# Optimization experiments

Measured on AMD Instinct MI355X. Metric: run time of the kernel, lower is better.

Reference implementation:

```python
import jax, jax.numpy as jnp
import numpy as np

N, K, CIN, COUT = 150000, 27, 32, 64
EPS = 1e-5
NEG_SLOPE = 0.01


def setup_inputs() -> dict:
    key = jax.random.key(0)
    k1, k2, k3, k4, k5, k6 = jax.random.split(key, 6)
    feats = jax.random.normal(k1, (N, CIN), dtype=jnp.float32)
    nbr = jax.random.randint(k2, (N, K), 0, N, dtype=jnp.int32)
    mask = jax.random.randint(k3, (N, K), 0, 2, dtype=jnp.int32).astype(jnp.bool_)
    # per-offset conv weights [K, Cin, Cout], kaiming-ish scale
    W = jax.random.normal(k4, (K, CIN, COUT), dtype=jnp.float32) / np.sqrt(K * CIN)
    gamma = jax.random.normal(k5, (COUT,), dtype=jnp.float32) * 0.1 + 1.0
    beta = jax.random.normal(k6, (COUT,), dtype=jnp.float32) * 0.1
    return {"feats": feats, "W": W, "gamma": gamma, "beta": beta, "nbr": nbr, "mask": mask}


def reference(feats, W, gamma, beta, nbr, mask):
    # sparse conv as gather-GEMM-(implicit scatter): out[n] = sum_k W[k]^T f[nbr[n,k]]
    gathered = jnp.where(mask[..., None], feats[nbr], 0.0)          # [N, K, Cin]
    out = jnp.einsum('nkc,kcd->nd', gathered, W)                     # [N, Cout]
    # BatchNorm over voxel axis (training-mode batch stats)
    mean = jnp.mean(out, axis=0)
    var = jnp.var(out, axis=0)
    out = (out - mean) * jax.lax.rsqrt(var + EPS) * gamma + beta
    # LeakyReLU, negative_slope = 0.01
    return jnp.where(out >= 0, out, NEG_SLOPE * out)
```

## Files before the change

### kernel.cpp

```cpp
#include <hip/hip_runtime.h>

#define N_VOX  150000
#define KNBR   27
#define CIN    32
#define COUT   64
#define NBUCKET 64
#define NEG_SLOPE 0.01f
#define EPS 1e-5f
#define APPLY_BLOCKS 1024
#define VPB 256

typedef __bf16 bf16x8 __attribute__((ext_vector_type(8)));
typedef float  f32x4  __attribute__((ext_vector_type(4)));

#define NB_FEATS 2344
#define NB_W       27
#define NB_Z       32

__global__ __launch_bounds__(256) void prep_all(
    const float* __restrict__ feats, const float* __restrict__ W,
    __bf16* __restrict__ fb, __bf16* __restrict__ Wp,
    float* __restrict__ bsums)
{
    const int t = threadIdx.x;
    int b = blockIdx.x;

    if (b < NB_FEATS) {
        const int i = b * 256 + t;
        if (i < N_VOX * CIN / 8) {
            const float4* p = reinterpret_cast<const float4*>(feats) + (size_t)i * 2;
            const float4 a = p[0], c = p[1];
            bf16x8 o;
            o[0]=(__bf16)a.x; o[1]=(__bf16)a.y; o[2]=(__bf16)a.z; o[3]=(__bf16)a.w;
            o[4]=(__bf16)c.x; o[5]=(__bf16)c.y; o[6]=(__bf16)c.z; o[7]=(__bf16)c.w;
            reinterpret_cast<bf16x8*>(fb)[i] = o;
        }
        return;
    }
    b -= NB_FEATS;

    if (b < NB_W) {
        const int u = b * 256 + t;
        const int lane = u & 63, f = u >> 6;
        const int s = f & 3, k = f >> 2;
        const int n = lane & 15, q = lane >> 4;
        const float* src = W + ((size_t)(k * CIN + q * 8) * COUT + s * 16 + n);
        bf16x8 o;
#pragma unroll
        for (int j = 0; j < 8; ++j) o[j] = (__bf16)src[(size_t)j * COUT];
        reinterpret_cast<bf16x8*>(Wp)[u] = o;
        return;
    }
    b -= NB_W;

    const int z = b * 256 + t;
    if (z < NBUCKET * 2 * COUT) bsums[z] = 0.0f;
}

__global__ __launch_bounds__(256, 2) void conv_mfma5(
    const __bf16* __restrict__ fb,
    const __bf16* __restrict__ Wp,
    const int* __restrict__ nbr,
    const int* __restrict__ mask,
    float* __restrict__ out,
    float* __restrict__ bsums)
{
    __shared__ int idx_s[VPB * KNBR];

    const int t    = threadIdx.x;
    const int base = blockIdx.x * VPB;

    {
        const size_t gb = (size_t)base * KNBR;
        const int vlim  = N_VOX - base;
        const int ilim  = (vlim < VPB ? vlim : VPB) * KNBR;
#pragma unroll
        for (int j = 0; j < KNBR; ++j) {
            const int i = t + 256 * j;
            int v = -1;
            if (i < ilim) v = (mask[gb + i] != 0) ? nbr[gb + i] : -1;
            idx_s[i] = v;
        }
    }
    __syncthreads();

    const int wave = t >> 6;
    const int lane = t & 63;
    const int n16  = lane & 15;
    const int q    = lane >> 4;
    const int wb   = wave * 64;

    const bf16x8* __restrict__ bp = reinterpret_cast<const bf16x8*>(Wp);
    const bf16x8 zv = {};

    const int rr0 = (wb +  0 + n16) * KNBR;
    const int rr1 = (wb + 16 + n16) * KNBR;
    const int rr2 = (wb + 32 + n16) * KNBR;
    const int rr3 = (wb + 48 + n16) * KNBR;

    f32x4 acc[4][4];
#pragma unroll
    for (int a = 0; a < 4; ++a)
#pragma unroll
        for (int b2 = 0; b2 < 4; ++b2) acc[a][b2] = (f32x4){0.f,0.f,0.f,0.f};

    bf16x8 ga[3][4];
    bf16x8 bb[2][4];

#define STAGE_A(K, B) do { \
    const int _i0 = idx_s[rr0 + (K)]; \
    const int _i1 = idx_s[rr1 + (K)]; \
    const int _i2 = idx_s[rr2 + (K)]; \
    const int _i3 = idx_s[rr3 + (K)]; \
    ga[B][0] = *reinterpret_cast<const bf16x8*>(fb + (size_t)(_i0 < 0 ? 0 : _i0) * CIN + q * 8); \
    ga[B][1] = *reinterpret_cast<const bf16x8*>(fb + (size_t)(_i1 < 0 ? 0 : _i1) * CIN + q * 8); \
    ga[B][2] = *reinterpret_cast<const bf16x8*>(fb + (size_t)(_i2 < 0 ? 0 : _i2) * CIN + q * 8); \
    ga[B][3] = *reinterpret_cast<const bf16x8*>(fb + (size_t)(_i3 < 0 ? 0 : _i3) * CIN + q * 8); \
    if (_i0 < 0) ga[B][0] = zv; \
    if (_i1 < 0) ga[B][1] = zv; \
    if (_i2 < 0) ga[B][2] = zv; \
    if (_i3 < 0) ga[B][3] = zv; \
} while (0)

#define STAGE_B(K, B) do { \
    bb[B][0] = bp[((K) * 4 + 0) * 64 + lane]; \
    bb[B][1] = bp[((K) * 4 + 1) * 64 + lane]; \
    bb[B][2] = bp[((K) * 4 + 2) * 64 + lane]; \
    bb[B][3] = bp[((K) * 4 + 3) * 64 + lane]; \
} while (0)

    STAGE_A(0, 0);
    STAGE_B(0, 0);
    STAGE_A(1, 1);
    STAGE_A(2, 2);

#pragma unroll
    for (int k = 0; k < KNBR; ++k) {
        const int cb = k % 3;
        const int db = k & 1;
        if (k + 1 < KNBR) STAGE_B(k + 1, (k + 1) & 1);
#pragma unroll
        for (int s = 0; s < 4; ++s) {
            acc[0][s] = __builtin_amdgcn_mfma_f32_16x16x32_bf16(ga[cb][0], bb[db][s], acc[0][s], 0, 0, 0);
            acc[1][s] = __builtin_amdgcn_mfma_f32_16x16x32_bf16(ga[cb][1], bb[db][s], acc[1][s], 0, 0, 0);
            acc[2][s] = __builtin_amdgcn_mfma_f32_16x16x32_bf16(ga[cb][2], bb[db][s], acc[2][s], 0, 0, 0);
            acc[3][s] = __builtin_amdgcn_mfma_f32_16x16x32_bf16(ga[cb][3], bb[db][s], acc[3][s], 0, 0, 0);
        }
        if (k + 3 < KNBR) STAGE_A(k + 3, cb);
    }
#undef STAGE_A
#undef STAGE_B

#pragma unroll
    for (int sl = 0; sl < 4; ++sl) {
        const int orow_b = base + wb + sl * 16 + q * 4;
#pragma unroll
        for (int r = 0; r < 4; ++r) {
            const int orow = orow_b + r;
            if (orow < N_VOX) {
                float* dst = out + (size_t)orow * COUT + n16;
#pragma unroll
                for (int s = 0; s < 4; ++s) dst[s * 16] = acc[sl][s][r];
            }
        }
    }

    float* dstb = bsums + ((blockIdx.x * 4 + wave) & (NBUCKET - 1)) * (2 * COUT);
#pragma unroll
    for (int s = 0; s < 4; ++s) {
        float ps = 0.f, pq = 0.f;
#pragma unroll
        for (int sl = 0; sl < 4; ++sl)
#pragma unroll
            for (int r = 0; r < 4; ++r) {
                const float x = acc[sl][s][r];
                ps += x; pq += x * x;
            }
        ps += __shfl_down(ps, 32); ps += __shfl_down(ps, 16);
        pq += __shfl_down(pq, 32); pq += __shfl_down(pq, 16);
        if (q == 0) {
            atomicAdd(dstb + s * 16 + n16, ps);
            atomicAdd(dstb + COUT + s * 16 + n16, pq);
        }
    }
}

__global__ __launch_bounds__(256) void bn_stats_apply(
    float* __restrict__ out, const float* __restrict__ bsums,
    const float* __restrict__ gamma, const float* __restrict__ beta)
{
    __shared__ float s_sc[COUT], s_sh[COUT];
    const int t = threadIdx.x;
    if (t < COUT) {
        float s = 0.f, qq = 0.f;
#pragma unroll 8
        for (int b = 0; b < NBUCKET; ++b) {
            s  += bsums[b * (2 * COUT) + t];
            qq += bsums[b * (2 * COUT) + COUT + t];
        }
        const float inv_n = 1.0f / (float)N_VOX;
        const float mean  = s * inv_n;
        const float var   = qq * inv_n - mean * mean;
        const float scale = gamma[t] * rsqrtf(var + EPS);
        s_sc[t] = scale;
        s_sh[t] = beta[t] - mean * scale;
    }
    __syncthreads();

    const long total4 = (long)N_VOX * COUT / 4;
    const long stride = (long)APPLY_BLOCKS * 256;
    long i = (long)blockIdx.x * 256 + t;
    const int cg = (int)(i & 15);
    const float4 sc = reinterpret_cast<const float4*>(s_sc)[cg];
    const float4 sh = reinterpret_cast<const float4*>(s_sh)[cg];
    for (; i < total4; i += stride) {
        float4 v = reinterpret_cast<float4*>(out)[i];
        float x;
        x = fmaf(v.x, sc.x, sh.x); v.x = (x >= 0.f) ? x : NEG_SLOPE * x;
        x = fmaf(v.y, sc.y, sh.y); v.y = (x >= 0.f) ? x : NEG_SLOPE * x;
        x = fmaf(v.z, sc.z, sh.z); v.z = (x >= 0.f) ? x : NEG_SLOPE * x;
        x = fmaf(v.w, sc.w, sh.w); v.w = (x >= 0.f) ? x : NEG_SLOPE * x;
        reinterpret_cast<float4*>(out)[i] = v;
    }
}

#define TM 64
#define FS 68
__global__ __launch_bounds__(256) void conv_f32(
    const float* __restrict__ feats, const float* __restrict__ W,
    const int* __restrict__ nbr, const int* __restrict__ mask,
    float* __restrict__ out, float* __restrict__ bsums)
{
    __shared__ float f_s[CIN * FS];
    __shared__ float w_s[CIN * COUT];
    const int t = threadIdx.x;
    const int tx = t & 15, ty = t >> 4;
    const int base = blockIdx.x * TM;
    const int gr = t >> 2, cq = t & 3;
    const int n_g = base + gr;
    float acc[4][4];
#pragma unroll
    for (int i = 0; i < 4; ++i)
#pragma unroll
        for (int j = 0; j < 4; ++j) acc[i][j] = 0.0f;
    for (int k = 0; k < KNBR; ++k) {
        int idx = -1;
        if (n_g < N_VOX) {
            const long off = (long)n_g * KNBR + k;
            if (mask[off] != 0) idx = nbr[off];
        }
        float4 fa = make_float4(0.f, 0.f, 0.f, 0.f);
        float4 fbv = fa;
        if (idx >= 0) {
            const float4* fp = reinterpret_cast<const float4*>(feats + (long)idx * CIN + cq * 8);
            fa = fp[0]; fbv = fp[1];
        }
        const float4* wsrc = reinterpret_cast<const float4*>(W + (long)k * CIN * COUT + t * 8);
        const float4 wa = wsrc[0], wb = wsrc[1];
        __syncthreads();
        const int c0 = cq * 8;
        f_s[(c0 + 0) * FS + gr] = fa.x; f_s[(c0 + 1) * FS + gr] = fa.y;
        f_s[(c0 + 2) * FS + gr] = fa.z; f_s[(c0 + 3) * FS + gr] = fa.w;
        f_s[(c0 + 4) * FS + gr] = fbv.x; f_s[(c0 + 5) * FS + gr] = fbv.y;
        f_s[(c0 + 6) * FS + gr] = fbv.z; f_s[(c0 + 7) * FS + gr] = fbv.w;
        reinterpret_cast<float4*>(w_s + t * 8)[0] = wa;
        reinterpret_cast<float4*>(w_s + t * 8)[1] = wb;
        __syncthreads();
#pragma unroll
        for (int c = 0; c < CIN; ++c) {
            const float4 fv = *reinterpret_cast<const float4*>(&f_s[c * FS + ty * 4]);
            const float4 wv = *reinterpret_cast<const float4*>(&w_s[c * COUT + tx * 4]);
            const float fr[4] = {fv.x, fv.y, fv.z, fv.w};
            const float wr[4] = {wv.x, wv.y, wv.z, wv.w};
#pragma unroll
            for (int i = 0; i < 4; ++i)
#pragma unroll
                for (int j = 0; j < 4; ++j)
                    acc[i][j] = fmaf(fr[i], wr[j], acc[i][j]);
        }
    }
#pragma unroll
    for (int i = 0; i < 4; ++i) {
        const int n = base + ty * 4 + i;
        if (n < N_VOX)
            *reinterpret_cast<float4*>(out + (long)n * COUT + tx * 4) =
                make_float4(acc[i][0], acc[i][1], acc[i][2], acc[i][3]);
    }
    float psum[4], psq[4];
#pragma unroll
    for (int j = 0; j < 4; ++j) {
        psum[j] = acc[0][j] + acc[1][j] + acc[2][j] + acc[3][j];
        psq[j]  = acc[0][j] * acc[0][j] + acc[1][j] * acc[1][j]
                + acc[2][j] * acc[2][j] + acc[3][j] * acc[3][j];
    }
    __syncthreads();
    *reinterpret_cast<float4*>(&f_s[ty * 64 + tx * 4]) = make_float4(psum[0], psum[1], psum[2], psum[3]);
    *reinterpret_cast<float4*>(&w_s[ty * 64 + tx * 4]) = make_float4(psq[0], psq[1], psq[2], psq[3]);
    __syncthreads();
    if (t < COUT) {
        float s = 0.f, qq = 0.f;
#pragma unroll
        for (int g = 0; g < 16; ++g) { s += f_s[g * 64 + t]; qq += w_s[g * 64 + t]; }
        float* dst = bsums + (blockIdx.x & (NBUCKET - 1)) * (2 * COUT);
        atomicAdd(dst + t, s);
        atomicAdd(dst + COUT + t, qq);
    }
}

extern "C" void kernel_launch(void* const* d_in, const int* in_sizes, int n_in,
                              void* d_out, int out_size, void* d_ws, size_t ws_size,
                              hipStream_t stream) {
    const float* feats = (const float*)d_in[0];
    const float* W     = (const float*)d_in[1];
    const float* gamma = (const float*)d_in[2];
    const float* beta  = (const float*)d_in[3];
    const int* nbr     = (const int*)d_in[4];
    const int* mask    = (const int*)d_in[5];
    float* out = (float*)d_out;
    char* ws   = (char*)d_ws;

    const size_t fb_bytes = (size_t)N_VOX * CIN * sizeof(__bf16);
    const size_t wp_bytes = (size_t)KNBR * 4 * 64 * 8 * sizeof(__bf16);
    const size_t bs_bytes = (size_t)NBUCKET * 2 * COUT * sizeof(float);

    if (ws_size >= fb_bytes + wp_bytes + bs_bytes) {
        __bf16* fb   = (__bf16*)ws;
        __bf16* Wp   = (__bf16*)(ws + fb_bytes);
        float* bsums = (float*)(ws + fb_bytes + wp_bytes);
        prep_all<<<NB_FEATS + NB_W + NB_Z, 256, 0, stream>>>(feats, W, fb, Wp, bsums);
        conv_mfma5<<<(N_VOX + VPB - 1) / VPB, 256, 0, stream>>>(fb, Wp, nbr, mask, out, bsums);
        bn_stats_apply<<<APPLY_BLOCKS, 256, 0, stream>>>(out, bsums, gamma, beta);
    } else {
        float* bsums = (float*)ws;
        hipMemsetAsync(bsums, 0, bs_bytes, stream);
        conv_f32<<<(N_VOX + TM - 1) / TM, 256, 0, stream>>>(feats, W, nbr, mask, out, bsums);
        bn_stats_apply<<<APPLY_BLOCKS, 256, 0, stream>>>(out, bsums, gamma, beta);
    }
}
```

Measured before the change: 175.9 us.

## Gather fp32 features directly in conv kernel, drop bf16 feature prep pass

Removes the pre-pass that converted all features to bf16 and instead gathers fp32 rows directly, converting to bf16 in registers before the MFMA. Voxels per block are halved to 128 (two 16-row tiles per wave) and launch bounds raised to 4 blocks/CU for more occupancy and latency hiding. Prefetch depth drops from 3-stage A to 2-stage. This saves a full-array conversion kernel but doubles gather bytes per neighbor row (128B fp32 vs 64B bf16) with random access, and W fragments are now loaded per 32 rows instead of 64.

New measurement: 186.0 us. 1.06x slower.

```diff
diff --git a/kernel.cpp b/kernel.cpp
--- a/kernel.cpp
+++ b/kernel.cpp
@@ -8,36 +8,20 @@
 #define NEG_SLOPE 0.01f
 #define EPS 1e-5f
 #define APPLY_BLOCKS 1024
-#define VPB 256
+#define VPB 128
 
 typedef __bf16 bf16x8 __attribute__((ext_vector_type(8)));
 typedef float  f32x4  __attribute__((ext_vector_type(4)));
 
-#define NB_FEATS 2344
-#define NB_W       27
-#define NB_Z       32
-
-__global__ __launch_bounds__(256) void prep_all(
-    const float* __restrict__ feats, const float* __restrict__ W,
-    __bf16* __restrict__ fb, __bf16* __restrict__ Wp,
+#define NB_W 27
+#define NB_Z 32
+
+__global__ __launch_bounds__(256) void prep_w(
+    const float* __restrict__ W, __bf16* __restrict__ Wp,
     float* __restrict__ bsums)
 {
     const int t = threadIdx.x;
     int b = blockIdx.x;
-
-    if (b < NB_FEATS) {
-        const int i = b * 256 + t;
-        if (i < N_VOX * CIN / 8) {
-            const float4* p = reinterpret_cast<const float4*>(feats) + (size_t)i * 2;
-            const float4 a = p[0], c = p[1];
-            bf16x8 o;
-            o[0]=(__bf16)a.x; o[1]=(__bf16)a.y; o[2]=(__bf16)a.z; o[3]=(__bf16)a.w;
-            o[4]=(__bf16)c.x; o[5]=(__bf16)c.y; o[6]=(__bf16)c.z; o[7]=(__bf16)c.w;
-            reinterpret_cast<bf16x8*>(fb)[i] = o;
-        }
-        return;
-    }
-    b -= NB_FEATS;
 
     if (b < NB_W) {
         const int u = b * 256 + t;
@@ -57,8 +41,8 @@
     if (z < NBUCKET * 2 * COUT) bsums[z] = 0.0f;
 }
 
-__global__ __launch_bounds__(256, 2) void conv_mfma5(
-    const __bf16* __restrict__ fb,
+__global__ __launch_bounds__(256, 4) void conv_mfma6(
+    const float* __restrict__ feats,
     const __bf16* __restrict__ Wp,
     const int* __restrict__ nbr,
     const int* __restrict__ mask,
@@ -75,11 +59,13 @@
         const int vlim  = N_VOX - base;
         const int ilim  = (vlim < VPB ? vlim : VPB) * KNBR;
 #pragma unroll
-        for (int j = 0; j < KNBR; ++j) {
+        for (int j = 0; j < (VPB * KNBR + 255) / 256; ++j) {
             const int i = t + 256 * j;
-            int v = -1;
-            if (i < ilim) v = (mask[gb + i] != 0) ? nbr[gb + i] : -1;
-            idx_s[i] = v;
+            if (i < VPB * KNBR) {
+                int v = -1;
+                if (i < ilim) v = (mask[gb + i] != 0) ? nbr[gb + i] : -1;
+                idx_s[i] = v;
+            }
         }
     }
     __syncthreads();
@@ -88,71 +74,75 @@
     const int lane = t & 63;
     const int n16  = lane & 15;
     const int q    = lane >> 4;
-    const int wb   = wave * 64;
-
-    const bf16x8* __restrict__ bp = reinterpret_cast<const bf16x8*>(Wp);
-    const bf16x8 zv = {};
+    const int wb   = wave * 32;
 
     const int rr0 = (wb +  0 + n16) * KNBR;
     const int rr1 = (wb + 16 + n16) * KNBR;
-    const int rr2 = (wb + 32 + n16) * KNBR;
-    const int rr3 = (wb + 48 + n16) * KNBR;
-
-    f32x4 acc[4][4];
-#pragma unroll
-    for (int a = 0; a < 4; ++a)
-#pragma unroll
-        for (int b2 = 0; b2 < 4; ++b2) acc[a][b2] = (f32x4){0.f,0.f,0.f,0.f};
-
-    bf16x8 ga[3][4];
-    bf16x8 bb[2][4];
-
-#define STAGE_A(K, B) do { \
+
+    const bf16x8* __restrict__ bp = reinterpret_cast<const bf16x8*>(Wp);
+    const float4* __restrict__ f4 = reinterpret_cast<const float4*>(feats);
+    const bf16x8 zv = {};
+
+    f32x4 acc[2][4];
+#pragma unroll
+    for (int a = 0; a < 2; ++a)
+#pragma unroll
+        for (int b2 = 0; b2 < 4; ++b2) acc[a][b2] = (f32x4){0.f, 0.f, 0.f, 0.f};
+
+    float4 ax[2][2][2];
+    int    av[2][2];
+    bf16x8 Bf[2][4];
+
+#define LOAD_A(K, R) do { \
     const int _i0 = idx_s[rr0 + (K)]; \
     const int _i1 = idx_s[rr1 + (K)]; \
-    const int _i2 = idx_s[rr2 + (K)]; \
-    const int _i3 = idx_s[rr3 + (K)]; \
-    ga[B][0] = *reinterpret_cast<const bf16x8*>(fb + (size_t)(_i0 < 0 ? 0 : _i0) * CIN + q * 8); \
-    ga[B][1] = *reinterpret_cast<const bf16x8*>(fb + (size_t)(_i1 < 0 ? 0 : _i1) * CIN + q * 8); \
-    ga[B][2] = *reinterpret_cast<const bf16x8*>(fb + (size_t)(_i2 < 0 ? 0 : _i2) * CIN + q * 8); \
-    ga[B][3] = *reinterpret_cast<const bf16x8*>(fb + (size_t)(_i3 < 0 ? 0 : _i3) * CIN + q * 8); \
-    if (_i0 < 0) ga[B][0] = zv; \
-    if (_i1 < 0) ga[B][1] = zv; \
-    if (_i2 < 0) ga[B][2] = zv; \
-    if (_i3 < 0) ga[B][3] = zv; \
+    const size_t _o0 = (size_t)(_i0 < 0 ? 0 : _i0) * 8 + q * 2; \
+    const size_t _o1 = (size_t)(_i1 < 0 ? 0 : _i1) * 8 + q * 2; \
+    ax[R][0][0] = f4[_o0]; ax[R][0][1] = f4[_o0 + 1]; \
+    ax[R][1][0] = f4[_o1]; ax[R][1][1] = f4[_o1 + 1]; \
+    av[R][0] = _i0; av[R][1] = _i1; \
 } while (0)
 
-#define STAGE_B(K, B) do { \
-    bb[B][0] = bp[((K) * 4 + 0) * 64 + lane]; \
-    bb[B][1] = bp[((K) * 4 + 1) * 64 + lane]; \
-    bb[B][2] = bp[((K) * 4 + 2) * 64 + lane]; \
-    bb[B][3] = bp[((K) * 4 + 3) * 64 + lane]; \
+#define LOAD_B(K, R) do { \
+    Bf[R][0] = bp[((K) * 4 + 0) * 64 + lane]; \
+    Bf[R][1] = bp[((K) * 4 + 1) * 64 + lane]; \
+    Bf[R][2] = bp[((K) * 4 + 2) * 64 + lane]; \
+    Bf[R][3] = bp[((K) * 4 + 3) * 64 + lane]; \
 } while (0)
 
-    STAGE_A(0, 0);
-    STAGE_B(0, 0);
-    STAGE_A(1, 1);
-    STAGE_A(2, 2);
+    LOAD_A(0, 0);
+    LOAD_B(0, 0);
 
 #pragma unroll
     for (int k = 0; k < KNBR; ++k) {
-        const int cb = k % 3;
-        const int db = k & 1;
-        if (k + 1 < KNBR) STAGE_B(k + 1, (k + 1) & 1);
+        const int cur = k & 1;
+        if (k + 1 < KNBR) {
+            LOAD_A(k + 1, cur ^ 1);
+            LOAD_B(k + 1, cur ^ 1);
+        }
+        bf16x8 a0, a1;
+        a0[0] = (__bf16)ax[cur][0][0].x; a0[1] = (__bf16)ax[cur][0][0].y;
+        a0[2] = (__bf16)ax[cur][0][0].z; a0[3] = (__bf16)ax[cur][0][0].w;
+        a0[4] = (__bf16)ax[cur][0][1].x; a0[5] = (__bf16)ax[cur][0][1].y;
+        a0[6] = (__bf16)ax[cur][0][1].z; a0[7] = (__bf16)ax[cur][0][1].w;
+        a1[0] = (__bf16)ax[cur][1][0].x; a1[1] = (__bf16)ax[cur][1][0].y;
+        a1[2] = (__bf16)ax[cur][1][0].z; a1[3] = (__bf16)ax[cur][1][0].w;
+        a1[4] = (__bf16)ax[cur][1][1].x; a1[5] = (__bf16)ax[cur][1][1].y;
+        a1[6] = (__bf16)ax[cur][1][1].z; a1[7] = (__bf16)ax[cur][1][1].w;
+        if (av[cur][0] < 0) a0 = zv;
+        if (av[cur][1] < 0) a1 = zv;
+
 #pragma unroll
         for (int s = 0; s < 4; ++s) {
-            acc[0][s] = __builtin_amdgcn_mfma_f32_16x16x32_bf16(ga[cb][0], bb[db][s], acc[0][s], 0, 0, 0);
-            acc[1][s] = __builtin_amdgcn_mfma_f32_16x16x32_bf16(ga[cb][1], bb[db][s], acc[1][s], 0, 0, 0);
-            acc[2][s] = __builtin_amdgcn_mfma_f32_16x16x32_bf16(ga[cb][2], bb[db][s], acc[2][s], 0, 0, 0);
-            acc[3][s] = __builtin_amdgcn_mfma_f32_16x16x32_bf16(ga[cb][3], bb[db][s], acc[3][s], 0, 0, 0);
-        }
-        if (k + 3 < KNBR) STAGE_A(k + 3, cb);
-    }
-#undef STAGE_A
-#undef STAGE_B
-
-#pragma unroll
-    for (int sl = 0; sl < 4; ++sl) {
+            acc[0][s] = __builtin_amdgcn_mfma_f32_16x16x32_bf16(a0, Bf[cur][s], acc[0][s], 0, 0, 0);
+            acc[1][s] = __builtin_amdgcn_mfma_f32_16x16x32_bf16(a1, Bf[cur][s], acc[1][s], 0, 0, 0);
+        }
+    }
+#undef LOAD_A
+#undef LOAD_B
+
+#pragma unroll
+    for (int sl = 0; sl < 2; ++sl) {
         const int orow_b = base + wb + sl * 16 + q * 4;
 #pragma unroll
         for (int r = 0; r < 4; ++r) {
@@ -170,7 +160,7 @@
     for (int s = 0; s < 4; ++s) {
         float ps = 0.f, pq = 0.f;
 #pragma unroll
-        for (int sl = 0; sl < 4; ++sl)
+        for (int sl = 0; sl < 2; ++sl)
 #pragma unroll
             for (int r = 0; r < 4; ++r) {
                 const float x = acc[sl][s][r];
@@ -319,16 +309,14 @@
     float* out = (float*)d_out;
     char* ws   = (char*)d_ws;
 
-    const size_t fb_bytes = (size_t)N_VOX * CIN * sizeof(__bf16);
     const size_t wp_bytes = (size_t)KNBR * 4 * 64 * 8 * sizeof(__bf16);
     const size_t bs_bytes = (size_t)NBUCKET * 2 * COUT * sizeof(float);
 
-    if (ws_size >= fb_bytes + wp_bytes + bs_bytes) {
-        __bf16* fb   = (__bf16*)ws;
-        __bf16* Wp   = (__bf16*)(ws + fb_bytes);
-        float* bsums = (float*)(ws + fb_bytes + wp_bytes);
-        prep_all<<<NB_FEATS + NB_W + NB_Z, 256, 0, stream>>>(feats, W, fb, Wp, bsums);
-        conv_mfma5<<<(N_VOX + VPB - 1) / VPB, 256, 0, stream>>>(fb, Wp, nbr, mask, out, bsums);
+    if (ws_size >= wp_bytes + bs_bytes) {
+        __bf16* Wp   = (__bf16*)ws;
+        float* bsums = (float*)(ws + wp_bytes);
+        prep_w<<<NB_W + NB_Z, 256, 0, stream>>>(W, Wp, bsums);
+        conv_mfma6<<<(N_VOX + VPB - 1) / VPB, 256, 0, stream>>>(feats, Wp, nbr, mask, out, bsums);
         bn_stats_apply<<<APPLY_BLOCKS, 256, 0, stream>>>(out, bsums, gamma, beta);
     } else {
         float* bsums = (float*)ws;
```
